# Kernel optimization log

Measured on AMD Instinct MI355X. Metric: run time of the kernel, lower is better.

## Reference

```python
import jax, jax.numpy as jnp
from jax import lax
import numpy as np

B, C, L = 64, 32, 1549
HID = 256          # LSTM hidden per direction
NH, DK = 8, 64     # n_heads, d_k ; NH*DK = 2*HID = 512
D2 = 2 * HID


def setup_inputs() -> dict:
    key = jax.random.key(0)
    ks = jax.random.split(key, 32)
    r = lambda i, shape: jax.random.normal(ks[i], shape, jnp.float32) * 0.05
    inp = {"x": jax.random.normal(ks[0], (B, C, L), jnp.float32)}
    inp["conv_w"] = r(1, (C, C, 16))
    inp["conv_b"] = r(2, (C,))
    inp["bn_gamma"] = 1.0 + r(3, (C,))
    inp["bn_beta"] = r(4, (C,))
    inp["bn_mean"] = r(5, (C,))
    inp["bn_var"] = jax.random.uniform(ks[6], (C,), jnp.float32, 0.5, 1.5)
    names = [("W_ih0f", (4*HID, C)), ("W_hh0f", (4*HID, HID)), ("b0f", (4*HID,)),
             ("W_ih0b", (4*HID, C)), ("W_hh0b", (4*HID, HID)), ("b0b", (4*HID,)),
             ("W_ih1f", (4*HID, D2)), ("W_hh1f", (4*HID, HID)), ("b1f", (4*HID,)),
             ("W_ih1b", (4*HID, D2)), ("W_hh1b", (4*HID, HID)), ("b1b", (4*HID,)),
             ("Wq", (D2, D2)), ("bq", (D2,)), ("Wk", (D2, D2)), ("bk", (D2,)),
             ("Wv", (D2, D2)), ("bv", (D2,)), ("ln_g", (D2,)), ("ln_b", (D2,)),
             ("fc_w", (1, D2)), ("fc_b", (1,))]
    for j, (n, s) in enumerate(names):
        inp[n] = r(7 + j, s)
    inp["ln_g"] = 1.0 + inp["ln_g"]
    return inp


def _lstm_dir(xg, W_hh, reverse):
    # xg: [B,S,4H] precomputed input-to-gate projections (+biases); PyTorch gate order i,f,g,o
    if reverse:
        xg = xg[:, ::-1]
    Bq = xg.shape[0]
    H = W_hh.shape[1]
    def step(carry, g_t):
        h, c = carry
        g = g_t + h @ W_hh.T
        i, f, gg, o = jnp.split(g, 4, axis=-1)
        c = jax.nn.sigmoid(f) * c + jax.nn.sigmoid(i) * jnp.tanh(gg)
        h = jax.nn.sigmoid(o) * jnp.tanh(c)
        return (h, c), h
    init = (jnp.zeros((Bq, H), xg.dtype), jnp.zeros((Bq, H), xg.dtype))
    _, hs = lax.scan(step, init, jnp.swapaxes(xg, 0, 1))
    hs = jnp.swapaxes(hs, 0, 1)
    return hs[:, ::-1] if reverse else hs


def _bilstm(x, Wif, Whf, bf, Wib, Whb, bb):
    hf = _lstm_dir(jnp.einsum('bsd,gd->bsg', x, Wif) + bf, Whf, False)
    hb = _lstm_dir(jnp.einsum('bsd,gd->bsg', x, Wib) + bb, Whb, True)
    return jnp.concatenate([hf, hb], axis=-1)


def _forward(x, conv_w, conv_b, bn_gamma, bn_beta, bn_mean, bn_var,
             W_ih0f, W_hh0f, b0f, W_ih0b, W_hh0b, b0b,
             W_ih1f, W_hh1f, b1f, W_ih1b, W_hh1b, b1b,
             Wq, bq, Wk, bk, Wv, bv, ln_g, ln_b, fc_w, fc_b):
    # conv1d (k=16, pad=1) + BatchNorm (eval) + relu + maxpool(k=3, stride=3)
    h = lax.conv_general_dilated(x, conv_w, (1,), [(1, 1)],
                                 dimension_numbers=('NCH', 'OIH', 'NCH')) + conv_b[None, :, None]
    h = (h - bn_mean[None, :, None]) * jax.lax.rsqrt(bn_var[None, :, None] + 1e-5) \
        * bn_gamma[None, :, None] + bn_beta[None, :, None]
    h = jax.nn.relu(h)
    h = lax.reduce_window(h, -jnp.inf, lax.max, (1, 1, 3), (1, 1, 3), 'VALID')
    h = jnp.transpose(h, (0, 2, 1))            # [B, S, C]
    # 2-layer bidirectional LSTM (eval: inter-layer dropout inactive)
    out = _bilstm(h, W_ih0f, W_hh0f, b0f, W_ih0b, W_hh0b, b0b)
    out = _bilstm(out, W_ih1f, W_hh1f, b1f, W_ih1b, W_hh1b, b1b)   # [B, S, 512]
    Bq, S, _ = out.shape
    q = (out @ Wq.T + bq).reshape(Bq, S, NH, DK).transpose(0, 2, 1, 3)
    k = (out @ Wk.T + bk).reshape(Bq, S, NH, DK).transpose(0, 2, 1, 3)
    v = (out @ Wv.T + bv).reshape(Bq, S, NH, DK).transpose(0, 2, 1, 3)
    attn = jnp.einsum('bhsd,bhtd->bhst', q, k) / np.sqrt(DK)
    # NOTE: original uses nn.LogSoftmax(dim=1) -> log-softmax over the HEAD axis
    la = jax.nn.log_softmax(attn, axis=1)
    ctx = jnp.einsum('bhst,bhtd->bhsd', la, v)
    ctx = jnp.transpose(ctx, (0, 2, 1, 3)).reshape(Bq, S, D2)
    r = out + ctx
    mu = jnp.mean(r, axis=-1, keepdims=True)
    var = jnp.mean((r - mu) ** 2, axis=-1, keepdims=True)
    r = (r - mu) * jax.lax.rsqrt(var + 1e-5) * ln_g + ln_b
    pooled = jnp.mean(r, axis=1)               # len_reduction='mean'
    return pooled @ fc_w.T + fc_b              # [B, 1]


def reference(x, conv_w, conv_b, bn_gamma, bn_beta, bn_mean, bn_var,
              W_ih0f, W_hh0f, b0f, W_ih0b, W_hh0b, b0b,
              W_ih1f, W_hh1f, b1f, W_ih1b, W_hh1b, b1b,
              Wq, bq, Wk, bk, Wv, bv, ln_g, ln_b, fc_w, fc_b):
    return _forward(x, conv_w, conv_b, bn_gamma, bn_beta, bn_mean, bn_var,
                    W_ih0f, W_hh0f, b0f, W_ih0b, W_hh0b, b0b,
                    W_ih1f, W_hh1f, b1f, W_ih1b, W_hh1b, b1b,
                    Wq, bq, Wk, bk, Wv, bv, ln_g, ln_b, fc_w, fc_b)
```

## Files before the change

kernel.cpp:

```cpp
#include <hip/hip_runtime.h>
#include <hip/hip_bf16.h>
#include <math.h>

#define L_IN 1549
#define S_OUT 512

typedef __hip_bfloat16 bf16;
typedef __attribute__((ext_vector_type(8))) short bfrag;
typedef __attribute__((ext_vector_type(4))) float f32x4;

__device__ __forceinline__ float bfbits2f(unsigned short u) {
    union { unsigned int i; float f; } x;
    x.i = ((unsigned int)u) << 16;
    return x.f;
}
__device__ __forceinline__ unsigned short f2bfbits(float f) {
    union { float f; unsigned int i; } x; x.f = f;
    unsigned int lsb = (x.i >> 16) & 1;
    return (unsigned short)((x.i + 0x7fff + lsb) >> 16);
}

__device__ __forceinline__ float fast_sig(float x) {
    float e = __builtin_amdgcn_exp2f(-1.442695041f * x);
    return __builtin_amdgcn_rcpf(1.f + e);
}
__device__ __forceinline__ float fast_tanh(float x) {
    float e = __builtin_amdgcn_exp2f(2.885390082f * x);
    return 1.f - 2.f * __builtin_amdgcn_rcpf(1.f + e);
}

#if __has_builtin(__builtin_amdgcn_fdot2_f32_bf16)
typedef __attribute__((ext_vector_type(2))) __bf16 v2bf;
__device__ __forceinline__ float dot2bf(unsigned int w, unsigned int h, float c) {
    union { unsigned int u; v2bf v; } a, b;
    a.u = w; b.u = h;
    return __builtin_amdgcn_fdot2_f32_bf16(a.v, b.v, c, false);
}
#else
__device__ __forceinline__ float dot2bf(unsigned int w, unsigned int h, float c) {
    union { unsigned int i; float f; } w0, w1, h0, h1;
    w0.i = w << 16; w1.i = w & 0xffff0000u;
    h0.i = h << 16; h1.i = h & 0xffff0000u;
    return c + w0.f * h0.f + w1.f * h1.f;
}
#endif

__global__ __launch_bounds__(256) void conv_bn_pool(
    const float* __restrict__ x, const float* __restrict__ w,
    const float* __restrict__ cb, const float* __restrict__ gamma,
    const float* __restrict__ beta, const float* __restrict__ mean,
    const float* __restrict__ var, bf16* __restrict__ h0)
{
    int b  = blockIdx.y;
    int sg = blockIdx.x;
    __shared__ float xs[32][40];
    int tid = threadIdx.x;
    int base = sg * 24;
    for (int i = tid; i < 32 * 40; i += 256) {
        int ci = i / 40, dl = i % 40;
        int l = base - 1 + dl;
        xs[ci][dl] = (l >= 0 && l < L_IN) ? x[(size_t)(b * 32 + ci) * L_IN + l] : 0.f;
    }
    __syncthreads();
    int c = tid & 31, sl = tid >> 5;
    float scale = gamma[c] * rsqrtf(var[c] + 1e-5f);
    float shift = beta[c] - mean[c] * scale;
    float bias = cb[c];
    float acc0 = bias, acc1 = bias, acc2 = bias;
    int off0 = 3 * sl;
    for (int ci = 0; ci < 32; ++ci) {
        const float* wrp = w + (size_t)(c * 32 + ci) * 16;
        float4 w0 = *(const float4*)(wrp);
        float4 w1 = *(const float4*)(wrp + 4);
        float4 w2 = *(const float4*)(wrp + 8);
        float4 w3 = *(const float4*)(wrp + 12);
        float wk[16] = {w0.x, w0.y, w0.z, w0.w, w1.x, w1.y, w1.z, w1.w,
                        w2.x, w2.y, w2.z, w2.w, w3.x, w3.y, w3.z, w3.w};
        const float* xr = &xs[ci][off0];
        #pragma unroll
        for (int kk = 0; kk < 16; ++kk) {
            float xv0 = xr[kk];
            float xv1 = xr[kk + 1];
            float xv2 = xr[kk + 2];
            acc0 += xv0 * wk[kk];
            acc1 += xv1 * wk[kk];
            acc2 += xv2 * wk[kk];
        }
    }
    float y0 = fmaxf(acc0 * scale + shift, 0.f);
    float y1 = fmaxf(acc1 * scale + shift, 0.f);
    float y2 = fmaxf(acc2 * scale + shift, 0.f);
    float best = fmaxf(fmaxf(y0, y1), y2);
    int s = sg * 8 + sl;
    h0[((size_t)b * S_OUT + s) * 32 + c] = __float2bfloat16(best);
}

__global__ void pack_lstm4(
    const float* __restrict__ W0, const float* __restrict__ W1,
    const float* __restrict__ W2, const float* __restrict__ W3,
    unsigned int* __restrict__ outbase)
{
    int set = blockIdx.y;
    const float* W = (set == 0) ? W0 : (set == 1) ? W1 : (set == 2) ? W2 : W3;
    unsigned int* out = outbase + (size_t)set * 131072;
    int i = blockIdx.x * 256 + threadIdx.x;
    int kp, t, col;
    if (i < 102400) {
        kp = i >> 10; col = (i >> 9) & 1; t = i & 511;
    } else if (i < 116736) {
        int j = i - 102400;
        kp = 100 + (j >> 10); t = (j & 1023) >> 1; col = j & 1;
    } else {
        int j = i - 116736;
        kp = 114 + (j >> 10); t = (j & 1023) >> 1; col = j & 1;
    }
    int g = 2 * t + col;
    unsigned int lo = f2bfbits(W[(size_t)g * 256 + 2 * kp]);
    unsigned int hi = f2bfbits(W[(size_t)g * 256 + 2 * kp + 1]);
    out[i] = lo | (hi << 16);
}

__global__ __launch_bounds__(256) void pack_b7(
    const float* __restrict__ A0, const float* __restrict__ A1,
    const float* __restrict__ A2, const float* __restrict__ A3,
    const float* __restrict__ A4, const float* __restrict__ A5,
    const float* __restrict__ A6, unsigned short* __restrict__ out)
{
    int i = blockIdx.x * 256 + threadIdx.x;
    const float* src; int j;
    if      (i <   32768) { src = A0; j = i; }
    else if (i <   65536) { src = A1; j = i - 32768; }
    else if (i <  589824) { src = A2; j = i - 65536; }
    else if (i < 1114112) { src = A3; j = i - 589824; }
    else if (i < 1376256) { src = A4; j = i - 1114112; }
    else if (i < 1638400) { src = A5; j = i - 1376256; }
    else if (i < 1900544) { src = A6; j = i - 1638400; }
    else return;
    out[i] = f2bfbits(src[j]);
}

#define LDA 40
__global__ __launch_bounds__(256) void gemm_mfma(
    const bf16* __restrict__ A,
    const bf16* __restrict__ Bm0, const bf16* __restrict__ Bm1, const bf16* __restrict__ Bm2,
    const float* __restrict__ bs0, const float* __restrict__ bs1, const float* __restrict__ bs2,
    bf16* __restrict__ Cm0, bf16* __restrict__ Cm1, bf16* __restrict__ Cm2,
    int M, int N, int K)
{
    int nbn = N >> 7;
    int nbm = M >> 7;
    int lid = blockIdx.x;
    int xcd = lid & 7;
    int slot = lid >> 3;
    int bn = slot % nbn;
    int pair = xcd + 8 * (slot / nbn);
    int bm = pair % nbm;
    int z  = pair / nbm;

    const bf16* B = (z == 0) ? Bm0 : ((z == 1) ? Bm1 : Bm2);
    const float* bias = (z == 0) ? bs0 : ((z == 1) ? bs1 : bs2);
    bf16* C = (z == 0) ? Cm0 : ((z == 1) ? Cm1 : Cm2);

    __shared__ bf16 As[128 * LDA];
    __shared__ bf16 Bs[128 * LDA];

    int tid = threadIdx.x;
    int lane = tid & 63;
    int wave = tid >> 6;
    int wm = (wave >> 1) * 64;
    int wn = (wave & 1) * 64;

    int sr = tid >> 2;
    int sc = (tid & 3) * 8;
    const bf16* Ag = A + (size_t)(bm * 128 + sr) * K + sc;
    const bf16* Bg = B + (size_t)(bn * 128 + sr) * K + sc;

    int fm = lane & 15;
    int fk = (lane >> 4) * 8;

    f32x4 acc[4][4];
    #pragma unroll
    for (int i = 0; i < 4; ++i)
        #pragma unroll
        for (int j = 0; j < 4; ++j) acc[i][j] = (f32x4)(0.f);

    for (int k0 = 0; k0 < K; k0 += 32) {
        float4 a0 = *(const float4*)(Ag + k0);
        float4 a1 = *(const float4*)(Ag + (size_t)64 * K + k0);
        float4 b0 = *(const float4*)(Bg + k0);
        float4 b1 = *(const float4*)(Bg + (size_t)64 * K + k0);
        __syncthreads();
        *(float4*)(As + sr * LDA + sc)        = a0;
        *(float4*)(As + (sr + 64) * LDA + sc) = a1;
        *(float4*)(Bs + sr * LDA + sc)        = b0;
        *(float4*)(Bs + (sr + 64) * LDA + sc) = b1;
        __syncthreads();

        bfrag af[4], bfr[4];
        #pragma unroll
        for (int i = 0; i < 4; ++i)
            af[i] = *(const bfrag*)(As + (wm + i * 16 + fm) * LDA + fk);
        #pragma unroll
        for (int j = 0; j < 4; ++j)
            bfr[j] = *(const bfrag*)(Bs + (wn + j * 16 + fm) * LDA + fk);
        #pragma unroll
        for (int i = 0; i < 4; ++i)
            #pragma unroll
            for (int j = 0; j < 4; ++j)
                acc[i][j] = __builtin_amdgcn_mfma_f32_16x16x32_bf16(
                    af[i], bfr[j], acc[i][j], 0, 0, 0);
    }

    int rbase = (lane >> 4) * 4;
    #pragma unroll
    for (int j = 0; j < 4; ++j) {
        int n = bn * 128 + wn + j * 16 + (lane & 15);
        float bv = bias[n];
        #pragma unroll
        for (int i = 0; i < 4; ++i) {
            #pragma unroll
            for (int r = 0; r < 4; ++r) {
                int m = bm * 128 + wm + i * 16 + rbase + r;
                C[(size_t)m * N + n] = __float2bfloat16(acc[i][j][r] + bv);
            }
        }
    }
}

__global__ __launch_bounds__(512, 1) void lstm_reg(
    const bf16* __restrict__ xg_f, const bf16* __restrict__ xg_b,
    const unsigned int* __restrict__ Wl, bf16* __restrict__ out)
{
    int u = blockIdx.x;
    int b = u & 63, dir = u >> 6;
    const unsigned int* W = Wl + (size_t)dir * 131072;
    const bf16* xg = dir ? xg_b : xg_f;
    int t = threadIdx.x;

    __shared__ unsigned int lw[14336];
    __shared__ __align__(16) unsigned int hsb[2][128];
    __shared__ float gsh[1024];

    unsigned int wr[200];
    #pragma unroll
    for (int j = 0; j < 200; ++j) wr[j] = W[j * 512 + t];
    for (int i = t; i < 14336; i += 512) lw[i] = W[102400 + i];
    if (t < 128) { hsb[0][t] = 0u; }
    float cst = 0.f;
    __syncthreads();

    const unsigned int* Wst = W + 116736;
    int par = 0;
    unsigned short hb = 0;
    size_t oaddr = 0;
    bool have_out = false;

    for (int step = 0; step < 512; ++step) {
        int ts = dir ? (511 - step) : step;

        uint2 sw[14];
        #pragma unroll
        for (int s = 0; s < 14; ++s)
            sw[s] = *(const uint2*)(Wst + s * 1024 + 2 * t);
        unsigned int xv =
            *(const unsigned int*)(xg + ((size_t)b * 512 + ts) * 1024 + 2 * t);

        const unsigned int* hs = hsb[par];
        float a0 = 0.f, a1 = 0.f;
        #pragma unroll
        for (int q = 0; q < 32; ++q) {
            uint4 hv = *(const uint4*)&hs[q * 4];
            #pragma unroll
            for (int r = 0; r < 4; ++r) {
                int kp = q * 4 + r;
                unsigned int h2 = (&hv.x)[r];
                if (kp < 100) {
                    a0 = dot2bf(wr[kp * 2], h2, a0);
                    a1 = dot2bf(wr[kp * 2 + 1], h2, a1);
                } else if (kp < 114) {
                    uint2 wv = *(const uint2*)&lw[(kp - 100) * 1024 + 2 * t];
                    a0 = dot2bf(wv.x, h2, a0);
                    a1 = dot2bf(wv.y, h2, a1);
                } else {
                    a0 = dot2bf(sw[kp - 114].x, h2, a0);
                    a1 = dot2bf(sw[kp - 114].y, h2, a1);
                }
            }
        }
        a0 += bfbits2f((unsigned short)(xv & 0xffff));
        a1 += bfbits2f((unsigned short)(xv >> 16));

        *(float2*)&gsh[2 * t] = make_float2(a0, a1);
        __syncthreads();

        if (t < 256) {
            float gi = gsh[t], gf = gsh[256 + t], gg = gsh[512 + t], go = gsh[768 + t];
            float si = fast_sig(gi);
            float sf = fast_sig(gf);
            float so = fast_sig(go);
            cst = sf * cst + si * fast_tanh(gg);
            float h = so * fast_tanh(cst);
            hb = f2bfbits(h);
            ((unsigned short*)hsb[par ^ 1])[t] = hb;
            oaddr = ((size_t)b * 512 + ts) * 512 + dir * 256 + t;
            have_out = true;
        }
        __syncthreads();
        if (have_out) {
            *(unsigned short*)(out + oaddr) = hb;
            have_out = false;
        }
        par ^= 1;
    }
}

__global__ __launch_bounds__(256) void vt_transpose(
    const bf16* __restrict__ v, bf16* __restrict__ vt)
{
    __shared__ unsigned short tile[64 * 73];
    int b = blockIdx.z;
    int s0 = blockIdx.x * 64, n0 = blockIdx.y * 64;
    int tid = threadIdx.x;
    #pragma unroll
    for (int u = 0; u < 2; ++u) {
        int idx = tid + u * 256;
        int si = idx >> 3, nj = (idx & 7) << 3;
        bfrag val = *(const bfrag*)(v + ((size_t)(b * 512 + s0 + si)) * 512 + n0 + nj);
        #pragma unroll
        for (int jj = 0; jj < 8; ++jj)
            tile[(nj + jj) * 73 + si] = ((unsigned short*)&val)[jj];
    }
    __syncthreads();
    #pragma unroll
    for (int u = 0; u < 2; ++u) {
        int idx = tid + u * 256;
        int ni = idx >> 3, sj = (idx & 7) << 3;
        unsigned short outv[8];
        #pragma unroll
        for (int jj = 0; jj < 8; ++jj)
            outv[jj] = tile[ni * 73 + sj + jj];
        *(float4*)(vt + (size_t)b * 262144 + (size_t)(n0 + ni) * 512 + s0 + sj) =
            *(float4*)outv;
    }
}

__global__ __launch_bounds__(256, 2) void attention_mfma(
    const bf16* __restrict__ q, const bf16* __restrict__ k,
    const bf16* __restrict__ vt, bf16* r)
{
    int n_ = blockIdx.x;
    int xcd = n_ & 7;
    int slot = n_ >> 3;
    int b = xcd + ((slot >> 4) << 3);
    int s0 = (slot & 15) * 32;
    int tid = threadIdx.x;
    int wave = tid >> 6;
    int sw = wave & 1, dh = wave >> 1;
    int lane = tid & 63;
    int L15 = lane & 15, quad = lane >> 4;

    const bf16* qrow = q + ((size_t)(b * 512 + s0 + sw * 16 + L15)) * 512;
    bfrag qf[8][2];
    #pragma unroll
    for (int h = 0; h < 8; ++h) {
        qf[h][0] = *(const bfrag*)(qrow + h * 64 + quad * 8);
        qf[h][1] = *(const bfrag*)(qrow + h * 64 + 32 + quad * 8);
    }

    f32x4 ctxa[8][2];
    #pragma unroll
    for (int h = 0; h < 8; ++h) {
        ctxa[h][0] = (f32x4)(0.f);
        ctxa[h][1] = (f32x4)(0.f);
    }

    int tperm = ((L15 >> 2) << 3) + (L15 & 3);
    const bf16* kbase = k + (size_t)(b * 512) * 512;
    const bf16* vbase = vt + (size_t)b * 262144;

    for (int tc = 0; tc < 512; tc += 32) {
        f32x4 sa[8][2];
        #pragma unroll
        for (int h = 0; h < 8; ++h) {
            #pragma unroll
            for (int tile = 0; tile < 2; ++tile) {
                const bf16* krow = kbase
                    + (size_t)(tc + tile * 4 + tperm) * 512 + h * 64 + quad * 8;
                bfrag a0 = *(const bfrag*)(krow);
                bfrag a1 = *(const bfrag*)(krow + 32);
                f32x4 acc = __builtin_amdgcn_mfma_f32_16x16x32_bf16(
                    a0, qf[h][0], (f32x4)(0.f), 0, 0, 0);
                acc = __builtin_amdgcn_mfma_f32_16x16x32_bf16(
                    a1, qf[h][1], acc, 0, 0, 0);
                sa[h][tile] = acc;
            }
        }
        bfrag pf[8];
        #pragma unroll
        for (int tile = 0; tile < 2; ++tile) {
            #pragma unroll
            for (int rr = 0; rr < 4; ++rr) {
                float sc[8];
                float m = -1e30f;
                #pragma unroll
                for (int h = 0; h < 8; ++h) {
                    sc[h] = sa[h][tile][rr] * 0.125f;
                    m = fmaxf(m, sc[h]);
                }
                float sum = 0.f;
                #pragma unroll
                for (int h = 0; h < 8; ++h)
                    sum += __builtin_amdgcn_exp2f((sc[h] - m) * 1.442695041f);
                float lse = m + 0.6931471806f * __builtin_amdgcn_logf(sum);
                #pragma unroll
                for (int h = 0; h < 8; ++h)
                    ((unsigned short*)&pf[h])[tile * 4 + rr] = f2bfbits(sc[h] - lse);
            }
        }
        #pragma unroll
        for (int h = 0; h < 8; ++h) {
            #pragma unroll
            for (int dt = 0; dt < 2; ++dt) {
                int n = h * 64 + dh * 32 + dt * 16 + L15;
                bfrag vf = *(const bfrag*)(vbase + (size_t)n * 512 + tc + quad * 8);
                ctxa[h][dt] = __builtin_amdgcn_mfma_f32_16x16x32_bf16(
                    pf[h], vf, ctxa[h][dt], 0, 0, 0);
            }
        }
    }
    #pragma unroll
    for (int h = 0; h < 8; ++h) {
        #pragma unroll
        for (int dt = 0; dt < 2; ++dt) {
            int n = h * 64 + dh * 32 + dt * 16 + L15;
            #pragma unroll
            for (int rr = 0; rr < 4; ++rr) {
                size_t addr =
                    ((size_t)(b * 512 + s0 + sw * 16 + quad * 4 + rr)) * 512 + n;
                float o = __bfloat162float(r[addr]);
                r[addr] = __float2bfloat16(o + ctxa[h][dt][rr]);
            }
        }
    }
}

__global__ __launch_bounds__(512) void ln_pool_fc(
    const bf16* __restrict__ r, const float* __restrict__ g, const float* __restrict__ bt,
    const float* __restrict__ fcw, const float* __restrict__ fcb, float* __restrict__ out)
{
    int b = blockIdx.y;
    int s = blockIdx.x * 8 + (threadIdx.x >> 6);
    int lane = threadIdx.x & 63;
    int n0 = lane * 8;

    float gf[8];
    float btf = 0.f;
    #pragma unroll
    for (int j = 0; j < 8; ++j) {
        float fw = fcw[n0 + j];
        gf[j] = g[n0 + j] * fw;
        btf += bt[n0 + j] * fw;
    }

    bfrag rv = *(const bfrag*)(r + ((size_t)(b * 512 + s)) * 512 + n0);
    float v[8];
    float s1 = 0.f, s2 = 0.f;
    #pragma unroll
    for (int j = 0; j < 8; ++j) {
        v[j] = bfbits2f(((const unsigned short*)&rv)[j]);
        s1 += v[j];
        s2 += v[j] * v[j];
    }
    #pragma unroll
    for (int off = 32; off > 0; off >>= 1) {
        s1 += __shfl_xor(s1, off);
        s2 += __shfl_xor(s2, off);
    }
    float mu = s1 * (1.f / 512.f);
    float var = s2 * (1.f / 512.f) - mu * mu;
    float rs = rsqrtf(var + 1e-5f);

    float d = 0.f;
    #pragma unroll
    for (int j = 0; j < 8; ++j) d += (v[j] - mu) * gf[j];
    #pragma unroll
    for (int off = 32; off > 0; off >>= 1) {
        d += __shfl_down(d, off);
        btf += __shfl_down(btf, off);
    }
    if (lane == 0) {
        float val = d * rs * (1.f / 512.f);
        if (s == 0) val += btf + fcb[0];
        atomicAdd(out + b, val);
    }
}

extern "C" void kernel_launch(void* const* d_in, const int* in_sizes, int n_in,
                              void* d_out, int out_size, void* d_ws, size_t ws_size,
                              hipStream_t stream)
{
    (void)in_sizes; (void)n_in; (void)ws_size;
    const float* x      = (const float*)d_in[0];
    const float* conv_w = (const float*)d_in[1];
    const float* conv_b = (const float*)d_in[2];
    const float* bn_g   = (const float*)d_in[3];
    const float* bn_b   = (const float*)d_in[4];
    const float* bn_m   = (const float*)d_in[5];
    const float* bn_v   = (const float*)d_in[6];
    const float* W_ih0f = (const float*)d_in[7];
    const float* W_hh0f = (const float*)d_in[8];
    const float* b0f    = (const float*)d_in[9];
    const float* W_ih0b = (const float*)d_in[10];
    const float* W_hh0b = (const float*)d_in[11];
    const float* b0b    = (const float*)d_in[12];
    const float* W_ih1f = (const float*)d_in[13];
    const float* W_hh1f = (const float*)d_in[14];
    const float* b1f    = (const float*)d_in[15];
    const float* W_ih1b = (const float*)d_in[16];
    const float* W_hh1b = (const float*)d_in[17];
    const float* b1b    = (const float*)d_in[18];
    const float* Wq = (const float*)d_in[19];
    const float* bq = (const float*)d_in[20];
    const float* Wk = (const float*)d_in[21];
    const float* bk = (const float*)d_in[22];
    const float* Wv = (const float*)d_in[23];
    const float* bv = (const float*)d_in[24];
    const float* ln_g = (const float*)d_in[25];
    const float* ln_b = (const float*)d_in[26];
    const float* fc_w = (const float*)d_in[27];
    const float* fc_b = (const float*)d_in[28];
    float* out = (float*)d_out;

    char* ws = (char*)d_ws;
    bf16* xgf  = (bf16*)ws;
    bf16* xgb  = xgf + 33554432;
    bf16* out0 = (bf16*)(ws + 134217728);
    bf16* out1 = (bf16*)(ws + 167772160);
    bf16* h0   = (bf16*)(ws + 201326592);
    unsigned int* wl0 = (unsigned int*)(ws + 203423744);
    unsigned int* wl1 = wl0 + 262144;
    bf16* wpk  = (bf16*)(ws + 205520896);
    bf16* qb = xgf;
    bf16* kb = xgf + 16777216;
    bf16* vb = xgb;
    bf16* vtb = out0;

    hipMemsetAsync(d_out, 0, (size_t)out_size * sizeof(float), stream);

    pack_lstm4<<<dim3(512, 4), 256, 0, stream>>>(
        W_hh0f, W_hh0b, W_hh1f, W_hh1b, wl0);

    pack_b7<<<7424, 256, 0, stream>>>(
        W_ih0f, W_ih0b, W_ih1f, W_ih1b, Wq, Wk, Wv, (unsigned short*)wpk);

    conv_bn_pool<<<dim3(64, 64), 256, 0, stream>>>(
        x, conv_w, conv_b, bn_g, bn_b, bn_m, bn_v, h0);

    gemm_mfma<<<4096, 256, 0, stream>>>(
        h0, wpk, wpk + 32768, nullptr, b0f, b0b, nullptr, xgf, xgb, nullptr,
        32768, 1024, 32);

    lstm_reg<<<128, 512, 0, stream>>>(xgf, xgb, wl0, out0);

    gemm_mfma<<<4096, 256, 0, stream>>>(
        out0, wpk + 65536, wpk + 589824, nullptr, b1f, b1b, nullptr,
        xgf, xgb, nullptr, 32768, 1024, 512);

    lstm_reg<<<128, 512, 0, stream>>>(xgf, xgb, wl1, out1);

    gemm_mfma<<<3072, 256, 0, stream>>>(
        out1, wpk + 1114112, wpk + 1376256, wpk + 1638400, bq, bk, bv,
        qb, kb, vb, 32768, 512, 512);

    vt_transpose<<<dim3(8, 8, 64), 256, 0, stream>>>(vb, vtb);

    attention_mfma<<<1024, 256, 0, stream>>>(qb, kb, vtb, out1);

    ln_pool_fc<<<dim3(64, 64), 512, 0, stream>>>(out1, ln_g, ln_b, fc_w, fc_b, out);
}
```

Before: 2.722 ms.

## Use 1024 threads per LSTM block, one gate column per thread

The recurrent LSTM kernel goes from 512 threads, each computing two gate columns, to 1024 threads, each computing one. The packed weight layout changes to match, so every thread now keeps 100 register words instead of 200 and does half the dot products per step. This is meant to shorten the serial per-step chain by spreading the recurrence matmul over more lanes and easing register pressure. The cost is that barriers now synchronise 16 waves instead of 8 and per-thread work per step is smaller.

```diff
diff --git a/kernel.cpp b/kernel.cpp
--- a/kernel.cpp
+++ b/kernel.cpp
@@ -104,17 +104,16 @@
     const float* W = (set == 0) ? W0 : (set == 1) ? W1 : (set == 2) ? W2 : W3;
     unsigned int* out = outbase + (size_t)set * 131072;
     int i = blockIdx.x * 256 + threadIdx.x;
-    int kp, t, col;
+    int kp, g;
     if (i < 102400) {
-        kp = i >> 10; col = (i >> 9) & 1; t = i & 511;
+        kp = i >> 10; g = i & 1023;
     } else if (i < 116736) {
         int j = i - 102400;
-        kp = 100 + (j >> 10); t = (j & 1023) >> 1; col = j & 1;
+        kp = 100 + (j >> 10); g = j & 1023;
     } else {
         int j = i - 116736;
-        kp = 114 + (j >> 10); t = (j & 1023) >> 1; col = j & 1;
-    }
-    int g = 2 * t + col;
+        kp = 114 + (j >> 10); g = j & 1023;
+    }
     unsigned int lo = f2bfbits(W[(size_t)g * 256 + 2 * kp]);
     unsigned int hi = f2bfbits(W[(size_t)g * 256 + 2 * kp + 1]);
     out[i] = lo | (hi << 16);
@@ -227,7 +226,7 @@
     }
 }
 
-__global__ __launch_bounds__(512, 1) void lstm_reg(
+__global__ __launch_bounds__(1024, 1) void lstm_reg(
     const bf16* __restrict__ xg_f, const bf16* __restrict__ xg_b,
     const unsigned int* __restrict__ Wl, bf16* __restrict__ out)
 {
@@ -241,10 +240,10 @@
     __shared__ __align__(16) unsigned int hsb[2][128];
     __shared__ float gsh[1024];
 
-    unsigned int wr[200];
-    #pragma unroll
-    for (int j = 0; j < 200; ++j) wr[j] = W[j * 512 + t];
-    for (int i = t; i < 14336; i += 512) lw[i] = W[102400 + i];
+    unsigned int wr[100];
+    #pragma unroll
+    for (int j = 0; j < 100; ++j) wr[j] = W[j * 1024 + t];
+    for (int i = t; i < 14336; i += 1024) lw[i] = W[102400 + i];
     if (t < 128) { hsb[0][t] = 0u; }
     float cst = 0.f;
     __syncthreads();
@@ -258,15 +257,15 @@
     for (int step = 0; step < 512; ++step) {
         int ts = dir ? (511 - step) : step;
 
-        uint2 sw[14];
+        unsigned int sw[14];
         #pragma unroll
         for (int s = 0; s < 14; ++s)
-            sw[s] = *(const uint2*)(Wst + s * 1024 + 2 * t);
-        unsigned int xv =
-            *(const unsigned int*)(xg + ((size_t)b * 512 + ts) * 1024 + 2 * t);
+            sw[s] = Wst[s * 1024 + t];
+        unsigned short xvs =
+            *(const unsigned short*)(xg + ((size_t)b * 512 + ts) * 1024 + t);
 
         const unsigned int* hs = hsb[par];
-        float a0 = 0.f, a1 = 0.f;
+        float a0 = 0.f, e0 = 0.f;
         #pragma unroll
         for (int q = 0; q < 32; ++q) {
             uint4 hv = *(const uint4*)&hs[q * 4];
@@ -274,23 +273,20 @@
             for (int r = 0; r < 4; ++r) {
                 int kp = q * 4 + r;
                 unsigned int h2 = (&hv.x)[r];
+                float& d = (r & 1) ? e0 : a0;
                 if (kp < 100) {
-                    a0 = dot2bf(wr[kp * 2], h2, a0);
-                    a1 = dot2bf(wr[kp * 2 + 1], h2, a1);
+                    d = dot2bf(wr[kp], h2, d);
                 } else if (kp < 114) {
-                    uint2 wv = *(const uint2*)&lw[(kp - 100) * 1024 + 2 * t];
-                    a0 = dot2bf(wv.x, h2, a0);
-                    a1 = dot2bf(wv.y, h2, a1);
+                    d = dot2bf(lw[(kp - 100) * 1024 + t], h2, d);
                 } else {
-                    a0 = dot2bf(sw[kp - 114].x, h2, a0);
-                    a1 = dot2bf(sw[kp - 114].y, h2, a1);
+                    d = dot2bf(sw[kp - 114], h2, d);
                 }
             }
         }
-        a0 += bfbits2f((unsigned short)(xv & 0xffff));
-        a1 += bfbits2f((unsigned short)(xv >> 16));
-
-        *(float2*)&gsh[2 * t] = make_float2(a0, a1);
+        a0 += e0;
+        a0 += bfbits2f(xvs);
+
+        gsh[t] = a0;
         __syncthreads();
 
         if (t < 256) {
@@ -560,13 +556,13 @@
         h0, wpk, wpk + 32768, nullptr, b0f, b0b, nullptr, xgf, xgb, nullptr,
         32768, 1024, 32);
 
-    lstm_reg<<<128, 512, 0, stream>>>(xgf, xgb, wl0, out0);
+    lstm_reg<<<128, 1024, 0, stream>>>(xgf, xgb, wl0, out0);
 
     gemm_mfma<<<4096, 256, 0, stream>>>(
         out0, wpk + 65536, wpk + 589824, nullptr, b1f, b1b, nullptr,
         xgf, xgb, nullptr, 32768, 1024, 512);
 
-    lstm_reg<<<128, 512, 0, stream>>>(xgf, xgb, wl1, out1);
+    lstm_reg<<<128, 1024, 0, stream>>>(xgf, xgb, wl1, out1);
 
     gemm_mfma<<<3072, 256, 0, stream>>>(
         out1, wpk + 1114112, wpk + 1376256, wpk + 1638400, bq, bk, bv,
```

Result: slower. 3.149 ms (+15.7%).
